# Kernel optimization log

Hardware: AMD Instinct MI355X
Metric: run time of the kernel (lower is better)

Reference implementation:

```python
import jax, jax.numpy as jnp
import numpy as np

V = 32000   # shared src/trg vocab size
E = 128     # EMB_DIM
H = 256     # HID_DIM
B = 32      # batch
S = 64      # src len
T = 64      # trg len


def setup_inputs() -> dict:
    key = jax.random.key(0)
    ks = jax.random.split(key, 16)
    s = 0.05
    n = lambda k, shape: jax.random.normal(k, shape, dtype=jnp.float32) * s
    return {
        "src": jax.random.randint(ks[0], (B, S), 0, V),
        "trg": jax.random.randint(ks[1], (B, T), 0, V),
        "enc_emb": n(ks[2], (V, E)),
        "enc_Wih": n(ks[3], (4 * H, E)),
        "enc_Whh": n(ks[4], (4 * H, H)),
        "enc_b": n(ks[5], (4 * H,)),   # b_ih + b_hh fused
        "dec_emb": n(ks[6], (V, E)),
        "dec_Wih": n(ks[7], (4 * H, E)),
        "dec_Whh": n(ks[8], (4 * H, H)),
        "dec_b": n(ks[9], (4 * H,)),
        "fc_W": n(ks[10], (V, H)),
        "fc_b": n(ks[11], (V,)),
    }


def _lstm_scan(x_seq, h0, c0, Wih, Whh, b):
    # x_seq: [T, B, E]; PyTorch gate order: i, f, g, o
    def step(carry, x):
        h, c = carry
        gates = x @ Wih.T + h @ Whh.T + b          # [B, 4H]
        i, f, g, o = jnp.split(gates, 4, axis=-1)
        c = jax.nn.sigmoid(f) * c + jax.nn.sigmoid(i) * jnp.tanh(g)
        h = jax.nn.sigmoid(o) * jnp.tanh(c)
        return (h, c), h
    (h, c), hs = jax.lax.scan(step, (h0, c0), x_seq)
    return h, c, hs


def reference(src, trg, enc_emb, enc_Wih, enc_Whh, enc_b,
              dec_emb, dec_Wih, dec_Whh, dec_b, fc_W, fc_b):
    dtype = enc_emb.dtype
    h0 = jnp.zeros((B, H), dtype)
    c0 = jnp.zeros((B, H), dtype)

    # Encoder: embed src, run LSTM, keep final (hidden, cell)
    src_e = enc_emb[src].transpose(1, 0, 2)        # [S, B, E]
    h, c, _ = _lstm_scan(src_e, h0, c0, enc_Wih, enc_Whh, enc_b)

    # Decoder with teacher_forcing_ratio=1.0: input at step t is trg[:, t-1]
    dec_in = dec_emb[trg[:, :-1]].transpose(1, 0, 2)   # [T-1, B, E]
    _, _, hs = _lstm_scan(dec_in, h, c, dec_Wih, dec_Whh, dec_b)  # [T-1, B, H]

    logits = hs @ fc_W.T + fc_b                    # [T-1, B, V]
    # outputs[:, 0, :] stays zero as in the torch code
    outputs = jnp.concatenate(
        [jnp.zeros((1, B, fc_W.shape[0]), dtype), logits], axis=0)
    return outputs.transpose(1, 0, 2)              # [B, T, V]
```

## Files before the change

kernel.cpp:

```cpp
#include <hip/hip_runtime.h>


typedef _Float16 f16x2 __attribute__((ext_vector_type(2)));
typedef _Float16 f16x8 __attribute__((ext_vector_type(8)));
typedef short short8 __attribute__((ext_vector_type(8)));
typedef float f32x4 __attribute__((ext_vector_type(4)));
typedef unsigned long long u64;

#define DEV __device__ __forceinline__

static constexpr int Vv = 32000, Ee = 128, Hh = 256, Bb = 32, Ss = 64, Tt = 64;
static constexpr int G4 = 4 * Hh;
static constexpr int MR = (Tt - 1) * Bb;
static constexpr size_t OUT_BT = (size_t)Tt * Vv;

static constexpr size_t OFF_ENCPRE = 0;
static constexpr size_t OFF_DECPRE = OFF_ENCPRE + (size_t)Ss * Bb * G4 * 4;
static constexpr size_t OFF_WQE    = OFF_DECPRE + (size_t)(Tt - 1) * Bb * G4 * 4;
static constexpr size_t OFF_WQD    = OFF_WQE + (size_t)G4 * Hh * 2;
static constexpr size_t OFF_WPE    = OFF_WQD + (size_t)G4 * Hh * 2;
static constexpr size_t OFF_WPD    = OFF_WPE + (size_t)G4 * Ee * 4;
static constexpr size_t OFF_HW     = OFF_WPD + (size_t)G4 * Ee * 4;

DEV float sigm(float x) { return 1.0f / (1.0f + expf(-x)); }

DEV unsigned short f2bf(float x) {
  unsigned u = __float_as_uint(x);
  u = u + 0x7fffu + ((u >> 16) & 1u);
  return (unsigned short)(u >> 16);
}

DEV float dot2(unsigned wu, unsigned hu, float acc) {
  union { unsigned u; f16x2 v; } a, b;
  a.u = wu; b.u = hu;
#if __has_builtin(__builtin_amdgcn_fdot2)
  return __builtin_amdgcn_fdot2(a.v, b.v, acc, false);
#else
  return acc + (float)a.v.x * (float)b.v.x + (float)a.v.y * (float)b.v.y;
#endif
}

__global__ __launch_bounds__(256) void k_prep(
    const float* __restrict__ WhhE_s, const float* __restrict__ WhhD_s,
    const float* __restrict__ WihE_s, const float* __restrict__ WihD_s,
    _Float16* __restrict__ WqE, _Float16* __restrict__ WqD,
    float* __restrict__ WpE, float* __restrict__ WpD,
    u64* __restrict__ hword) {
  int blk = blockIdx.x, t = threadIdx.x;
  if (blk < 32) { hword[blk * 256 + t] = 0ull; return; }
  blk -= 32;
  if (blk < 256) {
    const float* src = (blk < 128) ? WhhE_s : WhhD_s;
    _Float16*    dst = (blk < 128) ? WqE : WqD;
    int u = (blk & 127) * 256 + t;
    int k8 = u >> 10, r = u & 1023;
    const float* sp = src + r * Hh + k8 * 8;
    f16x8 v;
#pragma unroll
    for (int e = 0; e < 8; ++e) v[e] = (_Float16)sp[e];
    *(f16x8*)&dst[(size_t)u * 8] = v;
    return;
  }
  blk -= 256;
  {
    const float* src = (blk < 128) ? WihE_s : WihD_s;
    float*       dst = (blk < 128) ? WpE : WpD;
    int u = (blk & 127) * 256 + t;
    int e4 = u >> 10, g = u & 1023;
    f32x4 v = *(const f32x4*)(src + g * Ee + e4 * 4);
    *(f32x4*)&dst[(size_t)u * 4] = v;
  }
}

__global__ __launch_bounds__(1024) void k_pre(
    const int* __restrict__ src, const int* __restrict__ trg,
    const float* __restrict__ enc_emb, const float* __restrict__ dec_emb,
    const float* __restrict__ WpE, const float* __restrict__ WpD,
    const float* __restrict__ enc_b, const float* __restrict__ dec_b,
    float* __restrict__ enc_pre, float* __restrict__ dec_pre) {
  int blk = blockIdx.x;
  int step = blk >> 2;
  int b0 = (blk & 3) * 8;
  bool enc = step < Ss;
  int ts = enc ? step : step - Ss;
  const int*   tok  = enc ? src : trg;
  const float* emb  = enc ? enc_emb : dec_emb;
  const float* Wp   = enc ? WpE : WpD;
  const float* bias = enc ? enc_b : dec_b;
  float* pre = enc ? (enc_pre + ((size_t)step * Bb + b0) * G4)
                   : (dec_pre + ((size_t)(step - Ss) * Bb + b0) * G4);

  __shared__ __align__(16) float xs[8][128];
  int tid = threadIdx.x;
  {
    int bl = tid >> 7, e = tid & 127;
    int token = tok[(b0 + bl) * 64 + ts];
    xs[bl][e] = emb[(size_t)token * Ee + e];
  }
  __syncthreads();

  int g = tid;
  float acc[8];
  float bv = bias[g];
#pragma unroll
  for (int bb = 0; bb < 8; ++bb) acc[bb] = bv;

  const f32x4* w4 = (const f32x4*)Wp;
  const f32x4(*x4)[32] = (const f32x4(*)[32])xs;
#pragma unroll 4
  for (int e4 = 0; e4 < 32; ++e4) {
    f32x4 w = w4[(size_t)e4 * G4 + g];
#pragma unroll
    for (int bb = 0; bb < 8; ++bb) {
      f32x4 xv = x4[bb][e4];
      acc[bb] += w.x * xv.x + w.y * xv.y + w.z * xv.z + w.w * xv.w;
    }
  }
#pragma unroll
  for (int bb = 0; bb < 8; ++bb) pre[(size_t)bb * G4 + g] = acc[bb];
}

__global__ __launch_bounds__(256, 1) void k_lstm3(
    const float* __restrict__ enc_pre, const float* __restrict__ dec_pre,
    const _Float16* __restrict__ WqE, const _Float16* __restrict__ WqD,
    u64* __restrict__ hword, unsigned short* __restrict__ hsb) {
  const int bid = blockIdx.x;
  const int j = bid >> 5, b = bid & 31;
  const int t = threadIdx.x;
  const int wv = t >> 6, l = t & 63;
  const int c_loc = l & 31, khalf = l >> 5;
  const int r_loc = wv * 32 + c_loc;
  const int row = wv * 256 + j * 32 + c_loc;

  __shared__ uint4 wlds[2][32][128];
  __shared__ unsigned hbits[128];
  __shared__ float gbuf[4][32];
  __shared__ float hstash[32];

  {
    const uint4* gE = (const uint4*)WqE + row;
    const uint4* gD = (const uint4*)WqD + row;
#pragma unroll 4
    for (int kk = 0; kk < 32; ++kk) wlds[0][kk][r_loc] = gE[(size_t)kk * G4];
#pragma unroll 4
    for (int kk = 0; kk < 32; ++kk) wlds[1][kk][r_loc] = gD[(size_t)kk * G4];
  }
  float c = 0.0f;
  __syncthreads();

  for (int step = 0; step < 127; ++step) {
    const bool enc = step < Ss;
    const float* pre = (enc ? enc_pre + (size_t)step * (Bb * G4)
                            : dec_pre + (size_t)(step - Ss) * (Bb * G4)) +
                       (size_t)b * G4;
    float pv = pre[row];

    if (t < 128) {
      if (step == 0) {
        hbits[t] = 0u;
      } else {
        const int p = t >> 4;
        if (p != j) {
          u64* base = hword + ((size_t)(step & 1) * 32 + b) * 128;
          u64* sp = base + p * 16 + 15;
          u64 s;
          do {
            s = __hip_atomic_load(sp, __ATOMIC_RELAXED, __HIP_MEMORY_SCOPE_AGENT);
          } while ((unsigned)(s >> 32) != (unsigned)step);
          u64 v;
          if ((t & 15) == 15) {
            v = s;
          } else {
            u64* wp = base + t;
            do {
              v = __hip_atomic_load(wp, __ATOMIC_RELAXED, __HIP_MEMORY_SCOPE_AGENT);
            } while ((unsigned)(v >> 32) != (unsigned)step);
          }
          hbits[t] = (unsigned)v;
        }
      }
    }
    __syncthreads();

    const uint4* wl = &wlds[enc ? 0 : 1][khalf * 16][0];
    const uint4* hv4 = (const uint4*)hbits;
    float a0 = 0.f, a1 = 0.f, a2 = 0.f, a3 = 0.f;
#pragma unroll
    for (int k8 = 0; k8 < 16; ++k8) {
      uint4 w8 = wl[k8 * 128 + r_loc];
      uint4 h8 = hv4[khalf * 16 + k8];
      a0 = dot2(w8.x, h8.x, a0);
      a1 = dot2(w8.y, h8.y, a1);
      a2 = dot2(w8.z, h8.z, a2);
      a3 = dot2(w8.w, h8.w, a3);
    }
    float acc = (a0 + a1) + (a2 + a3);
    acc += __shfl_xor(acc, 32, 64);
    if (l < 32) gbuf[wv][c_loc] = acc + pv;
    __syncthreads();

    if (t < 32) {
      float gi = gbuf[0][t], gf = gbuf[1][t], gg = gbuf[2][t], go = gbuf[3][t];
      c = sigm(gf) * c + sigm(gi) * tanhf(gg);
      float hn = sigm(go) * tanhf(c);
      hstash[t] = hn;
      if (!enc)
        hsb[((size_t)(step - Ss) * Bb + b) * Hh + j * 32 + t] = f2bf(hn);
      if ((t & 1) == 0) {
        union { _Float16 f; unsigned short u; } u0, u1;
        u0.f = (_Float16)hn;
        u1.f = (_Float16)hstash[t + 1];
        u64 wd = ((u64)(unsigned)(step + 1) << 32) |
                 ((unsigned)u1.u << 16) | (unsigned)u0.u;
        __hip_atomic_store(
            hword + ((size_t)((step + 1) & 1) * 32 + b) * 128 + j * 16 + (t >> 1),
            wd, __ATOMIC_RELAXED, __HIP_MEMORY_SCOPE_AGENT);
        hbits[j * 16 + (t >> 1)] = (unsigned)wd;
      }
    }
  }
}

__global__ __launch_bounds__(256) void k_fc(const unsigned short* __restrict__ hsb,
                                            const float* __restrict__ fcW,
                                            const float* __restrict__ fcb,
                                            float* __restrict__ out) {
  constexpr int LDB = 264;
  __shared__ __align__(16) unsigned short As[64 * LDB];
  __shared__ __align__(16) unsigned short Bs[64 * LDB];
  int n0 = blockIdx.x * 64;
  int tid = threadIdx.x;
  int lane = tid & 63, wave = tid >> 6;
  int l15 = lane & 15, q = lane >> 4;
  int msub = (wave & 1) * 32, nsub = (wave >> 1) * 32;

  {
    int idx = tid * 8;
    int zb = idx >> 6, off = idx & 63;
    float* zp = out + (size_t)zb * OUT_BT + n0 + off;
    f32x4 z = {};
    *(f32x4*)zp = z;
    *(f32x4*)(zp + 4) = z;
  }

#pragma unroll
  for (int r = 0; r < 8; ++r) {
    int vecid = tid + 256 * r;
    int i = vecid >> 5;
    int kk = (vecid & 31) * 8;
    const float* pb = fcW + (size_t)(n0 + i) * Hh + kk;
    short8 vb;
#pragma unroll
    for (int e = 0; e < 8; ++e) vb[e] = (short)f2bf(pb[e]);
    *(short8*)&Bs[i * LDB + kk] = vb;
  }
  float bv0 = fcb[n0 + nsub + l15];
  float bv1 = fcb[n0 + nsub + 16 + l15];

  for (int mt = 0; mt < 32; ++mt) {
    int m0 = mt * 64;
    __syncthreads();
#pragma unroll
    for (int r = 0; r < 8; ++r) {
      int vecid = tid + 256 * r;
      int i = vecid >> 5;
      int kk = (vecid & 31) * 8;
      int gm = m0 + i;
      short8 va = {};
      if (gm < MR) va = *(const short8*)&hsb[(size_t)gm * Hh + kk];
      *(short8*)&As[i * LDB + kk] = va;
    }
    __syncthreads();

    f32x4 acc[2][2] = {};
#pragma unroll
    for (int ks = 0; ks < 8; ++ks) {
      int koff = ks * 32 + q * 8;
      short8 a0 = *(const short8*)&As[(msub + l15) * LDB + koff];
      short8 a1 = *(const short8*)&As[(msub + 16 + l15) * LDB + koff];
      short8 b0 = *(const short8*)&Bs[(nsub + l15) * LDB + koff];
      short8 b1 = *(const short8*)&Bs[(nsub + 16 + l15) * LDB + koff];
      acc[0][0] = __builtin_amdgcn_mfma_f32_16x16x32_bf16(a0, b0, acc[0][0], 0, 0, 0);
      acc[0][1] = __builtin_amdgcn_mfma_f32_16x16x32_bf16(a0, b1, acc[0][1], 0, 0, 0);
      acc[1][0] = __builtin_amdgcn_mfma_f32_16x16x32_bf16(a1, b0, acc[1][0], 0, 0, 0);
      acc[1][1] = __builtin_amdgcn_mfma_f32_16x16x32_bf16(a1, b1, acc[1][1], 0, 0, 0);
    }
#pragma unroll
    for (int ni = 0; ni < 2; ++ni) {
      int gn = n0 + nsub + ni * 16 + l15;
      float bv = ni ? bv1 : bv0;
#pragma unroll
      for (int mi = 0; mi < 2; ++mi) {
#pragma unroll
        for (int r = 0; r < 4; ++r) {
          int gm = m0 + msub + mi * 16 + q * 4 + r;
          if (gm < MR) {
            int tt = gm >> 5, bb = gm & 31;
            out[(size_t)bb * OUT_BT + (size_t)(tt + 1) * Vv + gn] = acc[mi][ni][r] + bv;
          }
        }
      }
    }
  }
}

extern "C" void kernel_launch(void* const* d_in, const int* in_sizes, int n_in,
                              void* d_out, int out_size, void* d_ws, size_t ws_size,
                              hipStream_t stream) {
  const int*   src     = (const int*)d_in[0];
  const int*   trg     = (const int*)d_in[1];
  const float* enc_emb = (const float*)d_in[2];
  const float* enc_Wih = (const float*)d_in[3];
  const float* enc_Whh = (const float*)d_in[4];
  const float* enc_b   = (const float*)d_in[5];
  const float* dec_emb = (const float*)d_in[6];
  const float* dec_Wih = (const float*)d_in[7];
  const float* dec_Whh = (const float*)d_in[8];
  const float* dec_b   = (const float*)d_in[9];
  const float* fc_W    = (const float*)d_in[10];
  const float* fc_b    = (const float*)d_in[11];
  float* out = (float*)d_out;

  char* ob = (char*)d_out;
  float*     enc_pre = (float*)(ob + OFF_ENCPRE);
  float*     dec_pre = (float*)(ob + OFF_DECPRE);
  _Float16*  WqE     = (_Float16*)(ob + OFF_WQE);
  _Float16*  WqD     = (_Float16*)(ob + OFF_WQD);
  float*     WpE     = (float*)(ob + OFF_WPE);
  float*     WpD     = (float*)(ob + OFF_WPD);
  u64*       hword   = (u64*)(ob + OFF_HW);
  unsigned short* hsb = (unsigned short*)d_ws;

  k_prep<<<544, 256, 0, stream>>>(enc_Whh, dec_Whh, enc_Wih, dec_Wih,
                                  WqE, WqD, WpE, WpD, hword);
  k_pre<<<508, 1024, 0, stream>>>(src, trg, enc_emb, dec_emb, WpE, WpD,
                                  enc_b, dec_b, enc_pre, dec_pre);
  k_lstm3<<<256, 256, 0, stream>>>(enc_pre, dec_pre, WqE, WqD, hword, hsb);
  k_fc<<<dim3(500), 256, 0, stream>>>(hsb, fc_W, fc_b, out);
}
```

Measured before the change: 637.3 us.

## Hold recurrent LSTM weights in registers and poll each h word directly

The persistent LSTM kernel now keeps each thread's slice of the recurrent fp16 weights in 16 uint4 registers, reloaded once per encoder and decoder phase, instead of reading them from LDS every step. A large dummy LDS array keeps the kernel at one block per CU. The cross-block h exchange drops the sentinel-word poll and instead polls each word directly, with three loads kept in flight. This targets LDS traffic and barrier latency on the serial 127-step critical path, at the cost of higher register pressure and extra polling traffic.

```diff
diff --git a/kernel.cpp b/kernel.cpp
--- a/kernel.cpp
+++ b/kernel.cpp
@@ -120,7 +120,7 @@
   for (int bb = 0; bb < 8; ++bb) pre[(size_t)bb * G4 + g] = acc[bb];
 }
 
-__global__ __launch_bounds__(256, 1) void k_lstm3(
+__global__ __launch_bounds__(256, 1) void k_lstm4(
     const float* __restrict__ enc_pre, const float* __restrict__ dec_pre,
     const _Float16* __restrict__ WqE, const _Float16* __restrict__ WqD,
     u64* __restrict__ hword, unsigned short* __restrict__ hsb) {
@@ -129,93 +129,82 @@
   const int t = threadIdx.x;
   const int wv = t >> 6, l = t & 63;
   const int c_loc = l & 31, khalf = l >> 5;
-  const int r_loc = wv * 32 + c_loc;
   const int row = wv * 256 + j * 32 + c_loc;
 
-  __shared__ uint4 wlds[2][32][128];
   __shared__ unsigned hbits[128];
   __shared__ float gbuf[4][32];
   __shared__ float hstash[32];
-
-  {
-    const uint4* gE = (const uint4*)WqE + row;
-    const uint4* gD = (const uint4*)WqD + row;
-#pragma unroll 4
-    for (int kk = 0; kk < 32; ++kk) wlds[0][kk][r_loc] = gE[(size_t)kk * G4];
-#pragma unroll 4
-    for (int kk = 0; kk < 32; ++kk) wlds[1][kk][r_loc] = gD[(size_t)kk * G4];
-  }
+  __shared__ uint4 lds_pad[7936];
+  if (hsb == nullptr) lds_pad[0] = uint4{0u, 0u, 0u, 0u};
+
   float c = 0.0f;
-  __syncthreads();
-
-  for (int step = 0; step < 127; ++step) {
-    const bool enc = step < Ss;
-    const float* pre = (enc ? enc_pre + (size_t)step * (Bb * G4)
-                            : dec_pre + (size_t)(step - Ss) * (Bb * G4)) +
-                       (size_t)b * G4;
-    float pv = pre[row];
-
-    if (t < 128) {
-      if (step == 0) {
-        hbits[t] = 0u;
-      } else {
-        const int p = t >> 4;
-        if (p != j) {
-          u64* base = hword + ((size_t)(step & 1) * 32 + b) * 128;
-          u64* sp = base + p * 16 + 15;
-          u64 s;
-          do {
-            s = __hip_atomic_load(sp, __ATOMIC_RELAXED, __HIP_MEMORY_SCOPE_AGENT);
-          } while ((unsigned)(s >> 32) != (unsigned)step);
-          u64 v;
-          if ((t & 15) == 15) {
-            v = s;
-          } else {
-            u64* wp = base + t;
-            do {
-              v = __hip_atomic_load(wp, __ATOMIC_RELAXED, __HIP_MEMORY_SCOPE_AGENT);
-            } while ((unsigned)(v >> 32) != (unsigned)step);
+
+  for (int phase = 0; phase < 2; ++phase) {
+    const uint4* gw = ((phase == 0) ? (const uint4*)WqE : (const uint4*)WqD)
+                      + (size_t)(khalf * 16) * G4 + row;
+    uint4 w[16];
+#pragma unroll
+    for (int i = 0; i < 16; ++i) w[i] = gw[(size_t)i * G4];
+
+    const int s0 = phase ? Ss : 0;
+    const int s1 = phase ? 127 : Ss;
+    const float* pbase = phase ? dec_pre : enc_pre;
+
+    for (int step = s0; step < s1; ++step) {
+      const float* pre = pbase + (size_t)(step - s0) * (Bb * G4) + (size_t)b * G4;
+      float pv = pre[row];
+
+      if (t < 128) {
+        if (step == 0) {
+          hbits[t] = 0u;
+        } else if ((t >> 4) != j) {
+          u64* wp = hword + ((size_t)(step & 1) * 32 + b) * 128 + t;
+          u64 v0 = __hip_atomic_load(wp, __ATOMIC_RELAXED, __HIP_MEMORY_SCOPE_AGENT);
+          u64 v1 = __hip_atomic_load(wp, __ATOMIC_RELAXED, __HIP_MEMORY_SCOPE_AGENT);
+          u64 v2 = __hip_atomic_load(wp, __ATOMIC_RELAXED, __HIP_MEMORY_SCOPE_AGENT);
+          while ((unsigned)(v0 >> 32) != (unsigned)step) {
+            v0 = v1; v1 = v2;
+            v2 = __hip_atomic_load(wp, __ATOMIC_RELAXED, __HIP_MEMORY_SCOPE_AGENT);
           }
-          hbits[t] = (unsigned)v;
+          hbits[t] = (unsigned)v0;
         }
       }
-    }
-    __syncthreads();
-
-    const uint4* wl = &wlds[enc ? 0 : 1][khalf * 16][0];
-    const uint4* hv4 = (const uint4*)hbits;
-    float a0 = 0.f, a1 = 0.f, a2 = 0.f, a3 = 0.f;
-#pragma unroll
-    for (int k8 = 0; k8 < 16; ++k8) {
-      uint4 w8 = wl[k8 * 128 + r_loc];
-      uint4 h8 = hv4[khalf * 16 + k8];
-      a0 = dot2(w8.x, h8.x, a0);
-      a1 = dot2(w8.y, h8.y, a1);
-      a2 = dot2(w8.z, h8.z, a2);
-      a3 = dot2(w8.w, h8.w, a3);
-    }
-    float acc = (a0 + a1) + (a2 + a3);
-    acc += __shfl_xor(acc, 32, 64);
-    if (l < 32) gbuf[wv][c_loc] = acc + pv;
-    __syncthreads();
-
-    if (t < 32) {
-      float gi = gbuf[0][t], gf = gbuf[1][t], gg = gbuf[2][t], go = gbuf[3][t];
-      c = sigm(gf) * c + sigm(gi) * tanhf(gg);
-      float hn = sigm(go) * tanhf(c);
-      hstash[t] = hn;
-      if (!enc)
-        hsb[((size_t)(step - Ss) * Bb + b) * Hh + j * 32 + t] = f2bf(hn);
-      if ((t & 1) == 0) {
-        union { _Float16 f; unsigned short u; } u0, u1;
-        u0.f = (_Float16)hn;
-        u1.f = (_Float16)hstash[t + 1];
-        u64 wd = ((u64)(unsigned)(step + 1) << 32) |
-                 ((unsigned)u1.u << 16) | (unsigned)u0.u;
-        __hip_atomic_store(
-            hword + ((size_t)((step + 1) & 1) * 32 + b) * 128 + j * 16 + (t >> 1),
-            wd, __ATOMIC_RELAXED, __HIP_MEMORY_SCOPE_AGENT);
-        hbits[j * 16 + (t >> 1)] = (unsigned)wd;
+      __syncthreads();
+
+      const uint4* hv4 = (const uint4*)hbits;
+      float a0 = 0.f, a1 = 0.f, a2 = 0.f, a3 = 0.f;
+#pragma unroll
+      for (int k8 = 0; k8 < 16; ++k8) {
+        uint4 w8 = w[k8];
+        uint4 h8 = hv4[khalf * 16 + k8];
+        a0 = dot2(w8.x, h8.x, a0);
+        a1 = dot2(w8.y, h8.y, a1);
+        a2 = dot2(w8.z, h8.z, a2);
+        a3 = dot2(w8.w, h8.w, a3);
+      }
+      float acc = (a0 + a1) + (a2 + a3);
+      acc += __shfl_xor(acc, 32, 64);
+      if (l < 32) gbuf[wv][c_loc] = acc + pv;
+      __syncthreads();
+
+      if (t < 32) {
+        float gi = gbuf[0][t], gf = gbuf[1][t], gg = gbuf[2][t], go = gbuf[3][t];
+        c = sigm(gf) * c + sigm(gi) * tanhf(gg);
+        float hn = sigm(go) * tanhf(c);
+        hstash[t] = hn;
+        if (phase)
+          hsb[((size_t)(step - Ss) * Bb + b) * Hh + j * 32 + t] = f2bf(hn);
+        if ((t & 1) == 0) {
+          union { _Float16 f; unsigned short u; } u0, u1;
+          u0.f = (_Float16)hn;
+          u1.f = (_Float16)hstash[t + 1];
+          u64 wd = ((u64)(unsigned)(step + 1) << 32) |
+                   ((unsigned)u1.u << 16) | (unsigned)u0.u;
+          __hip_atomic_store(
+              hword + ((size_t)((step + 1) & 1) * 32 + b) * 128 + j * 16 + (t >> 1),
+              wd, __ATOMIC_RELAXED, __HIP_MEMORY_SCOPE_AGENT);
+          hbits[j * 16 + (t >> 1)] = (unsigned)wd;
+        }
       }
     }
   }
@@ -335,6 +324,6 @@
                                   WqE, WqD, WpE, WpD, hword);
   k_pre<<<508, 1024, 0, stream>>>(src, trg, enc_emb, dec_emb, WpE, WpD,
                                   enc_b, dec_b, enc_pre, dec_pre);
-  k_lstm3<<<256, 256, 0, stream>>>(enc_pre, dec_pre, WqE, WqD, hword, hsb);
+  k_lstm4<<<256, 256, 0, stream>>>(enc_pre, dec_pre, WqE, WqD, hword, hsb);
   k_fc<<<dim3(500), 256, 0, stream>>>(hsb, fc_W, fc_b, out);
 }
```

Measured after the change: 665.9 us. +4.5%, slower.
